# Performance work log

Hardware: AMD Instinct MI355X
Metric: run time of the kernel (lower is better)

Reference implementation:

```python
import jax, jax.numpy as jnp
import numpy as np

CH = 256  # channels

def setup_inputs() -> dict:
    key = jax.random.key(0)
    ks = jax.random.split(key, 9)
    B, H, W = 8, 64, 64
    c8, c2 = CH // 8, CH // 2
    s = lambda fan_in: 1.0 / np.sqrt(fan_in)
    return {
        "x": jax.random.normal(ks[0], (B, H, W, CH), dtype=jnp.float32),
        "Wq": jax.random.normal(ks[1], (CH, c8), dtype=jnp.float32) * s(CH),
        "bq": jnp.zeros((c8,), dtype=jnp.float32),
        "Wk": jax.random.normal(ks[2], (CH, c8), dtype=jnp.float32) * s(CH),
        "bk": jnp.zeros((c8,), dtype=jnp.float32),
        "Wv": jax.random.normal(ks[3], (CH, c2), dtype=jnp.float32) * s(CH),
        "bv": jnp.zeros((c2,), dtype=jnp.float32),
        "Wo": jax.random.normal(ks[4], (c2, CH), dtype=jnp.float32) * s(c2),
        "bo": jnp.zeros((CH,), dtype=jnp.float32),
    }

def reference(x, Wq, bq, Wk, bk, Wv, bv, Wo, bo):
    B, H, W, C = x.shape
    # 1x1 convs are per-pixel matmuls over the channel dim
    q = x @ Wq + bq                      # [B,H,W,C/8]
    k = x @ Wk + bk                      # [B,H,W,C/8]
    v = x @ Wv + bv                      # [B,H,W,C/2]
    N = H * W
    qf = q.reshape(B, N, -1)
    kf = k.reshape(B, N, -1)
    vf = v.reshape(B, N, -1)
    # full self-attention over flattened spatial positions (no scaling, per source)
    scores = jnp.einsum('bnd,bmd->bnm', qf, kf)   # [B,N,N]
    attn = jax.nn.softmax(scores, axis=-1)
    out = jnp.einsum('bnm,bmd->bnd', attn, vf)    # [B,N,C/2]
    out = out.reshape(B, H, W, -1)
    return out @ Wo + bo + x
```

## Files before the change

### kernel.cpp

```cpp
#include <hip/hip_runtime.h>

typedef __attribute__((ext_vector_type(8))) short short8;
typedef __attribute__((ext_vector_type(8))) _Float16 half8;
typedef __attribute__((ext_vector_type(2))) float f32x2;
typedef __attribute__((ext_vector_type(4))) float f32x4;
typedef __attribute__((ext_vector_type(16))) float f32x16;

__device__ __forceinline__ unsigned short f2bf(float f) {
  unsigned int u = __float_as_uint(f);
  u += 0x7fffu + ((u >> 16) & 1u);
  return (unsigned short)(u >> 16);
}
__device__ __forceinline__ float bf2f(unsigned short h) {
  return __uint_as_float(((unsigned int)h) << 16);
}
__device__ __forceinline__ unsigned int cvtpk(float a, float b) {
  unsigned int r;
  asm("v_cvt_pk_bf16_f32 %0, %1, %2" : "=v"(r) : "v"(a), "v"(b));
  return r;
}
__device__ __forceinline__ unsigned short f2h(float f) {
  unsigned int r;
  asm("v_cvt_f16_f32 %0, %1" : "=v"(r) : "v"(f));
  return (unsigned short)r;
}
__device__ __forceinline__ float lo16f(unsigned int u) { return __uint_as_float(u << 16); }
__device__ __forceinline__ float hi16f(unsigned int u) { return __uint_as_float(u & 0xffff0000u); }
__device__ __forceinline__ short8 ld8(const unsigned short* p) {
  return *(const short8*)p;
}
__device__ __forceinline__ half8 ld8h(const unsigned short* p) {
  return *(const half8*)p;
}
__device__ __forceinline__ int swap23(int x) {
  return (x & 0x13) | ((x & 4) << 1) | ((x & 8) >> 1);
}
#define MFMA(a, b, c) __builtin_amdgcn_mfma_f32_16x16x32_bf16((a), (b), (c), 0, 0, 0)
#define MFMA32(a, b, c) __builtin_amdgcn_mfma_f32_32x32x16_bf16((a), (b), (c), 0, 0, 0)
#define MFMA32H(a, b, c) __builtin_amdgcn_mfma_f32_32x32x16_f16((a), (b), (c), 0, 0, 0)
#define LOG2E 1.4426950408889634f

typedef const __attribute__((address_space(1))) unsigned int* gas_u32p;
typedef __attribute__((address_space(3))) unsigned int* las_u32p;

__global__ void prep_weights(const float* __restrict__ Wq, const float* __restrict__ Wk,
                             const float* __restrict__ Wv, const float* __restrict__ Wo,
                             unsigned short* __restrict__ Wth, unsigned short* __restrict__ Wtl,
                             unsigned short* __restrict__ WoT) {
  int idx = blockIdx.x * 256 + threadIdx.x;
  if (idx < 192 * 256) {
    int o = idx >> 8, c = idx & 255;
    float w = (o < 32) ? Wq[c * 32 + o] : (o < 64) ? Wk[c * 32 + (o - 32)] : Wv[c * 128 + (o - 64)];
    unsigned short h = f2bf(w);
    Wth[idx] = h;
    Wtl[idx] = f2bf(w - bf2f(h));
  } else if (idx < 192 * 256 + 256 * 128) {
    int j = idx - 192 * 256;
    int c = j >> 7, d = j & 127;
    WoT[j] = f2bf(Wo[d * 256 + c]);
  }
}

__global__ __launch_bounds__(256) void proj_qkv(
    const float* __restrict__ x,
    const unsigned short* __restrict__ Wth, const unsigned short* __restrict__ Wtl,
    const float* __restrict__ bq, const float* __restrict__ bk, const float* __restrict__ bv,
    unsigned short* __restrict__ qh, unsigned short* __restrict__ KVF) {
  __shared__ unsigned short xsh[32][264];
  __shared__ unsigned short xsl[32][264];
  const int pix0 = blockIdx.x * 32;
  const int b = pix0 >> 12;
  const int nloc0 = pix0 & 4095;
  const int tid = threadIdx.x;

#pragma unroll
  for (int i = 0; i < 8; ++i) {
    int chunk = i * 256 + tid;
    int row = chunk >> 6;
    int c4 = (chunk & 63) * 4;
    float4 v = *(const float4*)(x + (size_t)(pix0 + row) * 256 + c4);
    unsigned int h01 = cvtpk(v.x, v.y), h23 = cvtpk(v.z, v.w);
    unsigned int l01 = cvtpk(v.x - lo16f(h01), v.y - hi16f(h01));
    unsigned int l23 = cvtpk(v.z - lo16f(h23), v.w - hi16f(h23));
    uint2 hp, lp;
    hp.x = h01; hp.y = h23;
    lp.x = l01; lp.y = l23;
    *(uint2*)&xsh[row][c4] = hp;
    *(uint2*)&xsl[row][c4] = lp;
  }
  __syncthreads();

  const int wave = tid >> 6, lane = tid & 63, l = lane & 15, qd = lane >> 4;
  const int nt = nloc0 >> 6;
  const int ktc = (nloc0 >> 5) & 1;
  const int ksbase = (nloc0 >> 4) & 2;
  const int hh = qd >> 1;
  const int eb = 4 * (qd & 1);

#pragma unroll
  for (int si = 0; si < 3; ++si) {
    const int sub = wave + si * 4;
    const int outc0 = sub * 16;
    if (si == 0) {
      const float* bp = (outc0 < 32) ? (bq + outc0) : (bk + outc0 - 32);
      const float4 bb = *(const float4*)(bp + 4 * qd);
      f32x4 acc[2];
      acc[0] = (f32x4){bb.x, bb.y, bb.z, bb.w};
      acc[1] = (f32x4){bb.x, bb.y, bb.z, bb.w};
#pragma unroll
      for (int kc = 0; kc < 8; ++kc) {
        short8 whf = ld8(Wth + (size_t)(outc0 + l) * 256 + kc * 32 + qd * 8);
        short8 wlf = ld8(Wtl + (size_t)(outc0 + l) * 256 + kc * 32 + qd * 8);
#pragma unroll
        for (int m = 0; m < 2; ++m) {
          short8 xhf = ld8(&xsh[m * 16 + l][kc * 32 + qd * 8]);
          short8 xlf = ld8(&xsl[m * 16 + l][kc * 32 + qd * 8]);
          acc[m] = MFMA(wlf, xhf, acc[m]);
          acc[m] = MFMA(whf, xlf, acc[m]);
          acc[m] = MFMA(whf, xhf, acc[m]);
        }
      }
      if (outc0 < 32) {
#pragma unroll
        for (int m = 0; m < 2; ++m) {
          const size_t pixel = (size_t)pix0 + m * 16 + l;
          uint2 st;
          st.x = (unsigned int)f2h(acc[m][0] * LOG2E) |
                 ((unsigned int)f2h(acc[m][1] * LOG2E) << 16);
          st.y = (unsigned int)f2h(acc[m][2] * LOG2E) |
                 ((unsigned int)f2h(acc[m][3] * LOG2E) << 16);
          *(uint2*)(qh + pixel * 32 + outc0 + 4 * qd) = st;
        }
      } else {
        const int step = (outc0 - 32) >> 4;
#pragma unroll
        for (int m = 0; m < 2; ++m) {
          const int lpos = swap23(m * 16 + l);
          const size_t koff = (size_t)(b * 64 + nt) * 10240 +
                              (ktc * 2 + step) * 512 + (hh * 32 + lpos) * 8 + eb;
          uint2 st;
          st.x = (unsigned int)f2h(acc[m][0]) | ((unsigned int)f2h(acc[m][1]) << 16);
          st.y = (unsigned int)f2h(acc[m][2]) | ((unsigned int)f2h(acc[m][3]) << 16);
          *(uint2*)(KVF + koff) = st;
        }
      }
    } else {
      const int dv = (outc0 - 64) + l;
      const float bias = bv[dv];
      f32x4 acc[2];
      acc[0] = (f32x4){bias, bias, bias, bias};
      acc[1] = (f32x4){bias, bias, bias, bias};
#pragma unroll
      for (int kc = 0; kc < 8; ++kc) {
        short8 whf = ld8(Wth + (size_t)(outc0 + l) * 256 + kc * 32 + qd * 8);
#pragma unroll
        for (int m = 0; m < 2; ++m) {
          short8 xhf = ld8(&xsh[m * 16 + l][kc * 32 + qd * 8]);
          acc[m] = MFMA(xhf, whf, acc[m]);
        }
      }
      const int dt = dv >> 5, lam = dv & 31;
#pragma unroll
      for (int m = 0; m < 2; ++m) {
        const int ks = ksbase + m;
        const size_t voff = (size_t)(b * 64 + nt) * 10240 + 2048 +
                            (dt * 4 + ks) * 512 + (hh * 32 + lam) * 8 + eb;
        uint2 st;
        st.x = cvtpk(acc[m][0], acc[m][1]);
        st.y = cvtpk(acc[m][2], acc[m][3]);
        *(uint2*)(KVF + voff) = st;
      }
    }
  }
}

__device__ __forceinline__ void stage_kv(const unsigned short* __restrict__ src,
                                         unsigned short* dst, int wave, int lane) {
#pragma unroll
  for (int i = 0; i < 5; ++i) {
    const int c = wave * 5 + i;
    __builtin_amdgcn_global_load_lds(
        (gas_u32p)(const void*)(src + c * 512 + lane * 8),
        (las_u32p)(void*)(dst + c * 512), 16, 0, 0);
  }
}

__global__ __launch_bounds__(256, 2) void flash_attn(
    const unsigned short* __restrict__ qh,
    const unsigned short* __restrict__ KVF, unsigned short* __restrict__ opart,
    float* __restrict__ lstat) {
  __shared__ unsigned short kv[2][10240];
  const int b = blockIdx.x & 7;
  const int r7 = blockIdx.x >> 3;
  const int tile = r7 & 15;
  const int split = r7 >> 4;
  const int wave = threadIdx.x >> 6;
  const int lane = threadIdx.x & 63;
  const int lam = lane & 31;
  const int h = lane >> 5;
  const int m0 = tile * 256 + wave * 64;
  const int nt0 = split * 16;

  const unsigned short* qh_b = qh + (size_t)b * 4096 * 32;
  const unsigned short* kv_b = KVF + (size_t)b * 64 * 10240;

  half8 qf[2][2];
#pragma unroll
  for (int t = 0; t < 2; ++t)
#pragma unroll
    for (int step = 0; step < 2; ++step)
      qf[t][step] = ld8h(qh_b + (size_t)(m0 + t * 32 + lam) * 32 + step * 16 + h * 8);

  f32x16 acc0[4], acc1[4];
#pragma unroll
  for (int dt = 0; dt < 4; ++dt)
#pragma unroll
    for (int e = 0; e < 16; ++e) { acc0[dt][e] = 0.f; acc1[dt][e] = 0.f; }
  f32x2 lr0 = (f32x2){0.f, 0.f}, lr1 = (f32x2){0.f, 0.f};

  stage_kv(kv_b + (size_t)nt0 * 10240, &kv[0][0], wave, lane);
  __syncthreads();

  int cur = 0;
#pragma unroll 1
  for (int it = 0; it < 16; ++it) {
    if (it < 15)
      stage_kv(kv_b + (size_t)(nt0 + it + 1) * 10240, &kv[cur ^ 1][0], wave, lane);

    const unsigned short* cb = &kv[cur][0];

    half8 k0a = ld8h(cb + 0 * 512 + lane * 8);
    half8 k0b = ld8h(cb + 1 * 512 + lane * 8);
    f32x16 z0, z1;
#pragma unroll
    for (int e = 0; e < 16; ++e) { z0[e] = 0.f; z1[e] = 0.f; }
    __builtin_amdgcn_s_setprio(1);
    z0 = MFMA32H(k0a, qf[0][0], z0);
    z0 = MFMA32H(k0b, qf[0][1], z0);
    z1 = MFMA32H(k0a, qf[1][0], z1);
    z1 = MFMA32H(k0b, qf[1][1], z1);
    __builtin_amdgcn_s_setprio(0);
    unsigned int ppA0[8], ppA1[8];
#pragma unroll
    for (int g = 0; g < 8; ++g) {
      float a0 = __builtin_amdgcn_exp2f(z0[2 * g]);
      float a1 = __builtin_amdgcn_exp2f(z0[2 * g + 1]);
      lr0 += (f32x2){a0, a1};
      ppA0[g] = cvtpk(a0, a1);
      float c0 = __builtin_amdgcn_exp2f(z1[2 * g]);
      float c1 = __builtin_amdgcn_exp2f(z1[2 * g + 1]);
      lr1 += (f32x2){c0, c1};
      ppA1[g] = cvtpk(c0, c1);
    }

    half8 k1a = ld8h(cb + 2 * 512 + lane * 8);
    half8 k1b = ld8h(cb + 3 * 512 + lane * 8);
    f32x16 w0, w1;
#pragma unroll
    for (int e = 0; e < 16; ++e) { w0[e] = 0.f; w1[e] = 0.f; }
    __builtin_amdgcn_s_setprio(1);
    w0 = MFMA32H(k1a, qf[0][0], w0);
    w0 = MFMA32H(k1b, qf[0][1], w0);
    w1 = MFMA32H(k1a, qf[1][0], w1);
    w1 = MFMA32H(k1b, qf[1][1], w1);
#pragma unroll
    for (int kss = 0; kss < 2; ++kss) {
      union { unsigned int u[4]; short8 v; } pf0, pf1;
#pragma unroll
      for (int j = 0; j < 4; ++j) { pf0.u[j] = ppA0[4 * kss + j]; pf1.u[j] = ppA1[4 * kss + j]; }
#pragma unroll
      for (int dt = 0; dt < 4; ++dt) {
        short8 vfrag = *(const short8*)(cb + 2048 + (dt * 4 + kss) * 512 + lane * 8);
        acc0[dt] = MFMA32(vfrag, pf0.v, acc0[dt]);
        acc1[dt] = MFMA32(vfrag, pf1.v, acc1[dt]);
      }
    }
    __builtin_amdgcn_s_setprio(0);
    unsigned int ppB0[8], ppB1[8];
#pragma unroll
    for (int g = 0; g < 8; ++g) {
      float a0 = __builtin_amdgcn_exp2f(w0[2 * g]);
      float a1 = __builtin_amdgcn_exp2f(w0[2 * g + 1]);
      lr0 += (f32x2){a0, a1};
      ppB0[g] = cvtpk(a0, a1);
      float c0 = __builtin_amdgcn_exp2f(w1[2 * g]);
      float c1 = __builtin_amdgcn_exp2f(w1[2 * g + 1]);
      lr1 += (f32x2){c0, c1};
      ppB1[g] = cvtpk(c0, c1);
    }
    __builtin_amdgcn_s_setprio(1);
#pragma unroll
    for (int kss = 0; kss < 2; ++kss) {
      union { unsigned int u[4]; short8 v; } pf0, pf1;
#pragma unroll
      for (int j = 0; j < 4; ++j) { pf0.u[j] = ppB0[4 * kss + j]; pf1.u[j] = ppB1[4 * kss + j]; }
#pragma unroll
      for (int dt = 0; dt < 4; ++dt) {
        short8 vfrag = *(const short8*)(cb + 2048 + (dt * 4 + 2 + kss) * 512 + lane * 8);
        acc0[dt] = MFMA32(vfrag, pf0.v, acc0[dt]);
        acc1[dt] = MFMA32(vfrag, pf1.v, acc1[dt]);
      }
    }
    __builtin_amdgcn_s_setprio(0);

    __syncthreads();
    cur ^= 1;
  }

  {
    const float lrun = lr0.x + lr0.y;
    const float ltot = lrun + __shfl_xor(lrun, 32);
    const int grow = b * 4096 + m0 + lam;
    if (h == 0) lstat[split * 32768 + grow] = ltot;
    const size_t obase = ((size_t)split * 32768 + grow) * 128;
#pragma unroll
    for (int dt = 0; dt < 4; ++dt)
#pragma unroll
      for (int g = 0; g < 8; ++g) {
        int r = 2 * g;
        int dv = dt * 32 + (r & 3) + 8 * (r >> 2) + 4 * h;
        *(unsigned int*)(opart + obase + dv) = cvtpk(acc0[dt][r], acc0[dt][r + 1]);
      }
  }
  {
    const float lrun = lr1.x + lr1.y;
    const float ltot = lrun + __shfl_xor(lrun, 32);
    const int grow = b * 4096 + m0 + 32 + lam;
    if (h == 0) lstat[split * 32768 + grow] = ltot;
    const size_t obase = ((size_t)split * 32768 + grow) * 128;
#pragma unroll
    for (int dt = 0; dt < 4; ++dt)
#pragma unroll
      for (int g = 0; g < 8; ++g) {
        int r = 2 * g;
        int dv = dt * 32 + (r & 3) + 8 * (r >> 2) + 4 * h;
        *(unsigned int*)(opart + obase + dv) = cvtpk(acc1[dt][r], acc1[dt][r + 1]);
      }
  }
}

__global__ __launch_bounds__(256) void combine_splits(
    const unsigned short* __restrict__ opart, const float* __restrict__ lstat,
    unsigned short* __restrict__ ao) {
  const int tid = threadIdx.x;
  const int row = blockIdx.x * 16 + (tid >> 4);
  const int col = (tid & 15) * 8;
  float den = lstat[row] + lstat[32768 + row] + lstat[65536 + row] + lstat[98304 + row];
  float inv = 1.f / den;
  float o[8] = {0.f, 0.f, 0.f, 0.f, 0.f, 0.f, 0.f, 0.f};
#pragma unroll
  for (int s = 0; s < 4; ++s) {
    uint4 v = *(const uint4*)(opart + ((size_t)s * 32768 + row) * 128 + col);
    unsigned int uu[4] = {v.x, v.y, v.z, v.w};
#pragma unroll
    for (int j = 0; j < 4; ++j) {
      o[2 * j]     += bf2f((unsigned short)(uu[j] & 0xffff));
      o[2 * j + 1] += bf2f((unsigned short)(uu[j] >> 16));
    }
  }
  uint4 outv;
  outv.x = cvtpk(o[0] * inv, o[1] * inv);
  outv.y = cvtpk(o[2] * inv, o[3] * inv);
  outv.z = cvtpk(o[4] * inv, o[5] * inv);
  outv.w = cvtpk(o[6] * inv, o[7] * inv);
  *(uint4*)(ao + (size_t)row * 128 + col) = outv;
}

__global__ __launch_bounds__(256) void out_proj(
    const unsigned short* __restrict__ ao, const unsigned short* __restrict__ WoT,
    const float* __restrict__ bo, const float* __restrict__ x, float* __restrict__ out) {
  const int pix0 = blockIdx.x * 64;
  const int wave = threadIdx.x >> 6, lane = threadIdx.x & 63, l = lane & 15, qd = lane >> 4;
  const int base = pix0 + wave * 16;
  short8 af[4];
#pragma unroll
  for (int kc = 0; kc < 4; ++kc)
    af[kc] = ld8(ao + (size_t)(base + l) * 128 + kc * 32 + qd * 8);
#pragma unroll
  for (int sub = 0; sub < 16; ++sub) {
    const int c0 = sub * 16 + 4 * qd;
    float4 bb = *(const float4*)(bo + c0);
    f32x4 acc = (f32x4){bb.x, bb.y, bb.z, bb.w};
#pragma unroll
    for (int kc = 0; kc < 4; ++kc) {
      short8 wf = ld8(WoT + (size_t)(sub * 16 + l) * 128 + kc * 32 + qd * 8);
      acc = MFMA(wf, af[kc], acc);
    }
    float4 xv = *(const float4*)(x + (size_t)(base + l) * 256 + c0);
    float4 res;
    res.x = acc[0] + xv.x;
    res.y = acc[1] + xv.y;
    res.z = acc[2] + xv.z;
    res.w = acc[3] + xv.w;
    *(float4*)(out + (size_t)(base + l) * 256 + c0) = res;
  }
}

__global__ __launch_bounds__(256) void combine_out(
    const unsigned short* __restrict__ opart, const float* __restrict__ lstat,
    const unsigned short* __restrict__ WoT,
    const float* __restrict__ bo, const float* __restrict__ x, float* __restrict__ out) {
  const int pix0 = blockIdx.x * 64;
  const int wave = threadIdx.x >> 6, lane = threadIdx.x & 63, l = lane & 15, qd = lane >> 4;
  const int base = pix0 + wave * 16;
  const int row = base + l;
  const float den = lstat[row] + lstat[32768 + row] + lstat[65536 + row] + lstat[98304 + row];
  const float inv = 1.f / den;
  short8 af[4];
#pragma unroll
  for (int kc = 0; kc < 4; ++kc) {
    float o[8] = {0.f, 0.f, 0.f, 0.f, 0.f, 0.f, 0.f, 0.f};
#pragma unroll
    for (int s = 0; s < 4; ++s) {
      uint4 v = *(const uint4*)(opart + ((size_t)s * 32768 + row) * 128 + kc * 32 + qd * 8);
      unsigned int uu[4] = {v.x, v.y, v.z, v.w};
#pragma unroll
      for (int j = 0; j < 4; ++j) {
        o[2 * j]     += bf2f((unsigned short)(uu[j] & 0xffff));
        o[2 * j + 1] += bf2f((unsigned short)(uu[j] >> 16));
      }
    }
    union { unsigned int u[4]; short8 v8; } pk;
#pragma unroll
    for (int j = 0; j < 4; ++j) pk.u[j] = cvtpk(o[2 * j] * inv, o[2 * j + 1] * inv);
    af[kc] = pk.v8;
  }
#pragma unroll
  for (int sub = 0; sub < 16; ++sub) {
    const int c0 = sub * 16 + 4 * qd;
    float4 bb = *(const float4*)(bo + c0);
    f32x4 acc = (f32x4){bb.x, bb.y, bb.z, bb.w};
#pragma unroll
    for (int kc = 0; kc < 4; ++kc) {
      short8 wf = ld8(WoT + (size_t)(sub * 16 + l) * 128 + kc * 32 + qd * 8);
      acc = MFMA(wf, af[kc], acc);
    }
    float4 xv = *(const float4*)(x + (size_t)row * 256 + c0);
    float4 res;
    res.x = acc[0] + xv.x;
    res.y = acc[1] + xv.y;
    res.z = acc[2] + xv.z;
    res.w = acc[3] + xv.w;
    *(float4*)(out + (size_t)row * 256 + c0) = res;
  }
}

extern "C" void kernel_launch(void* const* d_in, const int* in_sizes, int n_in,
                              void* d_out, int out_size, void* d_ws, size_t ws_size,
                              hipStream_t stream) {
  const float* x  = (const float*)d_in[0];
  const float* Wq = (const float*)d_in[1];
  const float* bq = (const float*)d_in[2];
  const float* Wk = (const float*)d_in[3];
  const float* bk = (const float*)d_in[4];
  const float* Wv = (const float*)d_in[5];
  const float* bv = (const float*)d_in[6];
  const float* Wo = (const float*)d_in[7];
  const float* bo = (const float*)d_in[8];

  char* ws = (char*)d_ws;
  unsigned short* qh  = (unsigned short*)(ws + 0);
  unsigned short* KVF = (unsigned short*)(ws + 2097152);
  unsigned short* Wth = (unsigned short*)(ws + 12582912);
  unsigned short* Wtl = (unsigned short*)(ws + 12681216);
  unsigned short* WoT = (unsigned short*)(ws + 12779520);
  float*          lst = (float*)(ws + 12845056);
  unsigned short* ao  = (unsigned short*)(ws + 13369344);

  const bool fused = (ws_size >= 50331648ull);
  unsigned short* opart = fused ? (unsigned short*)(ws + 16777216)
                                : (unsigned short*)d_out;

  prep_weights<<<320, 256, 0, stream>>>(Wq, Wk, Wv, Wo, Wth, Wtl, WoT);
  proj_qkv<<<1024, 256, 0, stream>>>(x, Wth, Wtl, bq, bk, bv, qh, KVF);
  flash_attn<<<512, 256, 0, stream>>>(qh, KVF, opart, lst);
  if (fused) {
    combine_out<<<512, 256, 0, stream>>>(opart, lst, WoT, bo, x, (float*)d_out);
  } else {
    combine_splits<<<2048, 256, 0, stream>>>(opart, lst, ao);
    out_proj<<<512, 256, 0, stream>>>(ao, WoT, bo, x, (float*)d_out);
  }
}
```

Baseline: 184.2 us.

## Halve per-wave query rows in flash attention to double grid and occupancy

Each wave now processes 32 query rows instead of 64, so the attention grid doubles to 1024 blocks. Launch bounds allow 4 blocks per CU. The aim is better latency hiding and CU utilisation through fewer accumulator registers and more resident waves. In exchange, each K/V tile staged into LDS is reused by half as many queries, which doubles K/V load traffic.

```diff
diff --git a/kernel.cpp b/kernel.cpp
--- a/kernel.cpp
+++ b/kernel.cpp
@@ -185,38 +185,36 @@
   }
 }
 
-__global__ __launch_bounds__(256, 2) void flash_attn(
+__global__ __launch_bounds__(256, 4) void flash_attn(
     const unsigned short* __restrict__ qh,
     const unsigned short* __restrict__ KVF, unsigned short* __restrict__ opart,
     float* __restrict__ lstat) {
   __shared__ unsigned short kv[2][10240];
   const int b = blockIdx.x & 7;
   const int r7 = blockIdx.x >> 3;
-  const int tile = r7 & 15;
-  const int split = r7 >> 4;
+  const int tile = r7 & 31;
+  const int split = r7 >> 5;
   const int wave = threadIdx.x >> 6;
   const int lane = threadIdx.x & 63;
   const int lam = lane & 31;
   const int h = lane >> 5;
-  const int m0 = tile * 256 + wave * 64;
+  const int m0 = tile * 128 + wave * 32;
   const int nt0 = split * 16;
 
   const unsigned short* qh_b = qh + (size_t)b * 4096 * 32;
   const unsigned short* kv_b = KVF + (size_t)b * 64 * 10240;
 
-  half8 qf[2][2];
-#pragma unroll
-  for (int t = 0; t < 2; ++t)
-#pragma unroll
-    for (int step = 0; step < 2; ++step)
-      qf[t][step] = ld8h(qh_b + (size_t)(m0 + t * 32 + lam) * 32 + step * 16 + h * 8);
-
-  f32x16 acc0[4], acc1[4];
+  half8 qf[2];
+#pragma unroll
+  for (int step = 0; step < 2; ++step)
+    qf[step] = ld8h(qh_b + (size_t)(m0 + lam) * 32 + step * 16 + h * 8);
+
+  f32x16 acc[4];
 #pragma unroll
   for (int dt = 0; dt < 4; ++dt)
 #pragma unroll
-    for (int e = 0; e < 16; ++e) { acc0[dt][e] = 0.f; acc1[dt][e] = 0.f; }
-  f32x2 lr0 = (f32x2){0.f, 0.f}, lr1 = (f32x2){0.f, 0.f};
+    for (int e = 0; e < 16; ++e) acc[dt][e] = 0.f;
+  f32x2 lr = (f32x2){0.f, 0.f};
 
   stage_kv(kv_b + (size_t)nt0 * 10240, &kv[0][0], wave, lane);
   __syncthreads();
@@ -231,74 +229,60 @@
 
     half8 k0a = ld8h(cb + 0 * 512 + lane * 8);
     half8 k0b = ld8h(cb + 1 * 512 + lane * 8);
-    f32x16 z0, z1;
-#pragma unroll
-    for (int e = 0; e < 16; ++e) { z0[e] = 0.f; z1[e] = 0.f; }
+    f32x16 z;
+#pragma unroll
+    for (int e = 0; e < 16; ++e) z[e] = 0.f;
     __builtin_amdgcn_s_setprio(1);
-    z0 = MFMA32H(k0a, qf[0][0], z0);
-    z0 = MFMA32H(k0b, qf[0][1], z0);
-    z1 = MFMA32H(k0a, qf[1][0], z1);
-    z1 = MFMA32H(k0b, qf[1][1], z1);
+    z = MFMA32H(k0a, qf[0], z);
+    z = MFMA32H(k0b, qf[1], z);
     __builtin_amdgcn_s_setprio(0);
-    unsigned int ppA0[8], ppA1[8];
+    unsigned int ppA[8];
 #pragma unroll
     for (int g = 0; g < 8; ++g) {
-      float a0 = __builtin_amdgcn_exp2f(z0[2 * g]);
-      float a1 = __builtin_amdgcn_exp2f(z0[2 * g + 1]);
-      lr0 += (f32x2){a0, a1};
-      ppA0[g] = cvtpk(a0, a1);
-      float c0 = __builtin_amdgcn_exp2f(z1[2 * g]);
-      float c1 = __builtin_amdgcn_exp2f(z1[2 * g + 1]);
-      lr1 += (f32x2){c0, c1};
-      ppA1[g] = cvtpk(c0, c1);
+      float a0 = __builtin_amdgcn_exp2f(z[2 * g]);
+      float a1 = __builtin_amdgcn_exp2f(z[2 * g + 1]);
+      lr += (f32x2){a0, a1};
+      ppA[g] = cvtpk(a0, a1);
     }
 
     half8 k1a = ld8h(cb + 2 * 512 + lane * 8);
     half8 k1b = ld8h(cb + 3 * 512 + lane * 8);
-    f32x16 w0, w1;
-#pragma unroll
-    for (int e = 0; e < 16; ++e) { w0[e] = 0.f; w1[e] = 0.f; }
+    f32x16 w;
+#pragma unroll
+    for (int e = 0; e < 16; ++e) w[e] = 0.f;
     __builtin_amdgcn_s_setprio(1);
-    w0 = MFMA32H(k1a, qf[0][0], w0);
-    w0 = MFMA32H(k1b, qf[0][1], w0);
-    w1 = MFMA32H(k1a, qf[1][0], w1);
-    w1 = MFMA32H(k1b, qf[1][1], w1);
+    w = MFMA32H(k1a, qf[0], w);
+    w = MFMA32H(k1b, qf[1], w);
 #pragma unroll
     for (int kss = 0; kss < 2; ++kss) {
-      union { unsigned int u[4]; short8 v; } pf0, pf1;
-#pragma unroll
-      for (int j = 0; j < 4; ++j) { pf0.u[j] = ppA0[4 * kss + j]; pf1.u[j] = ppA1[4 * kss + j]; }
+      union { unsigned int u[4]; short8 v; } pf;
+#pragma unroll
+      for (int j = 0; j < 4; ++j) pf.u[j] = ppA[4 * kss + j];
 #pragma unroll
       for (int dt = 0; dt < 4; ++dt) {
         short8 vfrag = *(const short8*)(cb + 2048 + (dt * 4 + kss) * 512 + lane * 8);
-        acc0[dt] = MFMA32(vfrag, pf0.v, acc0[dt]);
-        acc1[dt] = MFMA32(vfrag, pf1.v, acc1[dt]);
+        acc[dt] = MFMA32(vfrag, pf.v, acc[dt]);
       }
     }
     __builtin_amdgcn_s_setprio(0);
-    unsigned int ppB0[8], ppB1[8];
+    unsigned int ppB[8];
 #pragma unroll
     for (int g = 0; g < 8; ++g) {
-      float a0 = __builtin_amdgcn_exp2f(w0[2 * g]);
-      float a1 = __builtin_amdgcn_exp2f(w0[2 * g + 1]);
-      lr0 += (f32x2){a0, a1};
-      ppB0[g] = cvtpk(a0, a1);
-      float c0 = __builtin_amdgcn_exp2f(w1[2 * g]);
-      float c1 = __builtin_amdgcn_exp2f(w1[2 * g + 1]);
-      lr1 += (f32x2){c0, c1};
-      ppB1[g] = cvtpk(c0, c1);
+      float a0 = __builtin_amdgcn_exp2f(w[2 * g]);
+      float a1 = __builtin_amdgcn_exp2f(w[2 * g + 1]);
+      lr += (f32x2){a0, a1};
+      ppB[g] = cvtpk(a0, a1);
     }
     __builtin_amdgcn_s_setprio(1);
 #pragma unroll
     for (int kss = 0; kss < 2; ++kss) {
-      union { unsigned int u[4]; short8 v; } pf0, pf1;
-#pragma unroll
-      for (int j = 0; j < 4; ++j) { pf0.u[j] = ppB0[4 * kss + j]; pf1.u[j] = ppB1[4 * kss + j]; }
+      union { unsigned int u[4]; short8 v; } pf;
+#pragma unroll
+      for (int j = 0; j < 4; ++j) pf.u[j] = ppB[4 * kss + j];
 #pragma unroll
       for (int dt = 0; dt < 4; ++dt) {
         short8 vfrag = *(const short8*)(cb + 2048 + (dt * 4 + 2 + kss) * 512 + lane * 8);
-        acc0[dt] = MFMA32(vfrag, pf0.v, acc0[dt]);
-        acc1[dt] = MFMA32(vfrag, pf1.v, acc1[dt]);
+        acc[dt] = MFMA32(vfrag, pf.v, acc[dt]);
       }
     }
     __builtin_amdgcn_s_setprio(0);
@@ -307,36 +291,19 @@
     cur ^= 1;
   }
 
-  {
-    const float lrun = lr0.x + lr0.y;
-    const float ltot = lrun + __shfl_xor(lrun, 32);
-    const int grow = b * 4096 + m0 + lam;
-    if (h == 0) lstat[split * 32768 + grow] = ltot;
-    const size_t obase = ((size_t)split * 32768 + grow) * 128;
-#pragma unroll
-    for (int dt = 0; dt < 4; ++dt)
-#pragma unroll
-      for (int g = 0; g < 8; ++g) {
-        int r = 2 * g;
-        int dv = dt * 32 + (r & 3) + 8 * (r >> 2) + 4 * h;
-        *(unsigned int*)(opart + obase + dv) = cvtpk(acc0[dt][r], acc0[dt][r + 1]);
-      }
-  }
-  {
-    const float lrun = lr1.x + lr1.y;
-    const float ltot = lrun + __shfl_xor(lrun, 32);
-    const int grow = b * 4096 + m0 + 32 + lam;
-    if (h == 0) lstat[split * 32768 + grow] = ltot;
-    const size_t obase = ((size_t)split * 32768 + grow) * 128;
-#pragma unroll
-    for (int dt = 0; dt < 4; ++dt)
-#pragma unroll
-      for (int g = 0; g < 8; ++g) {
-        int r = 2 * g;
-        int dv = dt * 32 + (r & 3) + 8 * (r >> 2) + 4 * h;
-        *(unsigned int*)(opart + obase + dv) = cvtpk(acc1[dt][r], acc1[dt][r + 1]);
-      }
-  }
+  const float lrun = lr.x + lr.y;
+  const float ltot = lrun + __shfl_xor(lrun, 32);
+  const int grow = b * 4096 + m0 + lam;
+  if (h == 0) lstat[split * 32768 + grow] = ltot;
+  const size_t obase = ((size_t)split * 32768 + grow) * 128;
+#pragma unroll
+  for (int dt = 0; dt < 4; ++dt)
+#pragma unroll
+    for (int g = 0; g < 8; ++g) {
+      int r = 2 * g;
+      int dv = dt * 32 + (r & 3) + 8 * (r >> 2) + 4 * h;
+      *(unsigned int*)(opart + obase + dv) = cvtpk(acc[dt][r], acc[dt][r + 1]);
+    }
 }
 
 __global__ __launch_bounds__(256) void combine_splits(
@@ -473,7 +440,7 @@
 
   prep_weights<<<320, 256, 0, stream>>>(Wq, Wk, Wv, Wo, Wth, Wtl, WoT);
   proj_qkv<<<1024, 256, 0, stream>>>(x, Wth, Wtl, bq, bk, bv, qh, KVF);
-  flash_attn<<<512, 256, 0, stream>>>(qh, KVF, opart, lst);
+  flash_attn<<<1024, 256, 0, stream>>>(qh, KVF, opart, lst);
   if (fused) {
     combine_out<<<512, 256, 0, stream>>>(opart, lst, WoT, bo, x, (float*)d_out);
   } else {
```

Result: slower. 189.1 us (+2.7%).
